# Kernel tuning notes

Measured on AMD Instinct MI355X. Metric: run time of the kernel, lower is better.

The kernel has to match this reference:

```python
import jax, jax.numpy as jnp
import numpy as np

V, H, E, I, K = 32000, 1024, 8, 4096, 2  # vocab, hidden, experts, intermediate, top-k
B, S = 4, 512


def setup_inputs() -> dict:
    key = jax.random.key(0)
    ks = jax.random.split(key, 11)
    s = 0.02
    return {
        "input_ids": jax.random.randint(ks[0], (B, S), 0, V),
        "emb": jax.random.normal(ks[1], (V, H), dtype=jnp.float32) * s,
        "router_w": jax.random.normal(ks[2], (H, E), dtype=jnp.float32) * s,
        "router_b": jnp.zeros((E,), jnp.float32),
        "w1": jax.random.normal(ks[3], (E, H, I), dtype=jnp.float32) * s,
        "b1": jnp.zeros((E, I), jnp.float32),
        "w2": jax.random.normal(ks[4], (E, I, H), dtype=jnp.float32) * s,
        "b2": jnp.zeros((E, H), jnp.float32),
        "lm_w": jax.random.normal(ks[5], (H, V), dtype=jnp.float32) * s,
        "lm_b": jnp.zeros((V,), jnp.float32),
    }


def reference(input_ids, emb, router_w, router_b, w1, b1, w2, b2, lm_w, lm_b):
    b, s = input_ids.shape
    x = emb[input_ids].reshape(-1, H)                      # [T, H], T = b*s
    router_logits = x @ router_w + router_b                # [T, E]
    routing_weights, selected_experts = jax.lax.top_k(router_logits, K)
    routing_weights = jax.nn.softmax(routing_weights, axis=-1)  # [T, K]
    # NOTE: original torch code accumulates UNWEIGHTED expert outputs
    # (routing_weights never multiply expert_output). Faithfully reproduced.
    # mask[t, e] = 1 if expert e is in token t's top-k (top_k indices are distinct)
    mask = jnp.any(selected_experts[:, :, None] == jnp.arange(E)[None, None, :], axis=1)
    mask = mask.astype(x.dtype)                            # [T, E]
    # Dense dispatch: run every expert FFN on all tokens, then mask-combine.
    h = jax.nn.gelu(jnp.einsum('th,ehi->tei', x, w1) + b1, approximate=False)  # [T,E,I]
    y = jnp.einsum('tei,eih->teh', h, w2) + b2             # [T, E, H]
    expert_out = jnp.einsum('te,teh->th', mask, y)         # [T, H]
    hidden = expert_out.reshape(b, s, H)
    logits = hidden @ lm_w + lm_b                          # [B, S, V]
    return logits, routing_weights, selected_experts
```

## Files before the change

### kernel.cpp

```cpp
#include <hip/hip_runtime.h>
#include <math.h>

#define TT 2048
#define HH 1024
#define EE 8
#define II 4096
#define VV 32000

typedef __attribute__((ext_vector_type(8))) short short8;
typedef __attribute__((ext_vector_type(4))) float f32x4;
typedef __attribute__((ext_vector_type(4))) unsigned short us4;

__device__ __forceinline__ unsigned short f2bf(float f) {
  union { float f; unsigned u; } v; v.f = f;
  unsigned r = (v.u + 0x7FFFu + ((v.u >> 16) & 1u)) >> 16;
  return (unsigned short)r;
}

__device__ __forceinline__ void gl2lds16(const void* g, void* l) {
  __builtin_amdgcn_global_load_lds(
      (__attribute__((address_space(1))) void*)(g),
      (__attribute__((address_space(3))) void*)(l),
      16, 0, 0);
}

__global__ __launch_bounds__(256) void k_transpose(
    const float* __restrict__ in, unsigned short* __restrict__ out,
    int R, int C, size_t ibs, size_t obs)
{
  __shared__ unsigned short tl[64][72];
  const int tid = threadIdx.x;
  const int c0 = blockIdx.x * 64;
  const int r0 = blockIdx.y * 64;
  const float* ip = in + (size_t)blockIdx.z * ibs;
  unsigned short* op = out + (size_t)blockIdx.z * obs;
  const int rl = tid >> 4;
  const int cc = (tid & 15) * 4;
#pragma unroll
  for (int p = 0; p < 4; p++) {
    const float4 v = *(const float4*)&ip[(size_t)(r0 + p*16 + rl)*C + c0 + cc];
    tl[cc+0][p*16+rl] = f2bf(v.x);
    tl[cc+1][p*16+rl] = f2bf(v.y);
    tl[cc+2][p*16+rl] = f2bf(v.z);
    tl[cc+3][p*16+rl] = f2bf(v.w);
  }
  __syncthreads();
  const int cl = tid >> 2;
  const int hc = (tid & 3) * 16;
  int4* dst = (int4*)&op[(size_t)(c0 + cl)*R + r0 + hc];
  dst[0] = *(int4*)&tl[cl][hc];
  dst[1] = *(int4*)&tl[cl][hc + 8];
}

__global__ __launch_bounds__(64) void k_gather_router(
    const int* __restrict__ ids, const float* __restrict__ emb,
    const float* __restrict__ rw, const float* __restrict__ rb,
    unsigned short* __restrict__ xb, float* __restrict__ rweights,
    float* __restrict__ sel, int* __restrict__ counts, int* __restrict__ tok_list,
    int* __restrict__ tinfo)
{
  const int t = blockIdx.x;
  const int lane = threadIdx.x;
  const int tok = ids[t];
  float p[EE];
#pragma unroll
  for (int e = 0; e < EE; e++) p[e] = 0.f;
#pragma unroll
  for (int c = 0; c < 4; c++) {
    const int h = c*256 + lane*4;
    const float4 xv = *(const float4*)&emb[tok*HH + h];
    us4 u;
    u[0] = f2bf(xv.x); u[1] = f2bf(xv.y); u[2] = f2bf(xv.z); u[3] = f2bf(xv.w);
    *(us4*)&xb[t*HH + h] = u;
    const float xs[4] = {xv.x, xv.y, xv.z, xv.w};
#pragma unroll
    for (int j = 0; j < 4; j++) {
      const float4 r0 = *(const float4*)&rw[(h+j)*EE];
      const float4 r1 = *(const float4*)&rw[(h+j)*EE + 4];
      p[0] += xs[j]*r0.x; p[1] += xs[j]*r0.y; p[2] += xs[j]*r0.z; p[3] += xs[j]*r0.w;
      p[4] += xs[j]*r1.x; p[5] += xs[j]*r1.y; p[6] += xs[j]*r1.z; p[7] += xs[j]*r1.w;
    }
  }
#pragma unroll
  for (int off = 32; off >= 1; off >>= 1) {
#pragma unroll
    for (int e = 0; e < EE; e++) p[e] += __shfl_xor(p[e], off, 64);
  }
  if (lane == 0) {
#pragma unroll
    for (int e = 0; e < EE; e++) p[e] += rb[e];
    int b0 = 0; float v0 = p[0];
#pragma unroll
    for (int e = 1; e < EE; e++) { if (p[e] > v0) { v0 = p[e]; b0 = e; } }
    int b1 = -1; float v1 = -3.0e38f;
#pragma unroll
    for (int e = 0; e < EE; e++) { if (e != b0 && p[e] > v1) { v1 = p[e]; b1 = e; } }
    const float ex = expf(v1 - v0);
    const float w0 = 1.f / (1.f + ex);
    const float w1v = ex * w0;
    rweights[t*2]   = w0;
    rweights[t*2+1] = w1v;
    sel[t*2]   = (float)b0;
    sel[t*2+1] = (float)b1;
    int j0 = atomicAdd(&counts[b0], 1); tok_list[b0*TT + j0] = t;
    int j1 = atomicAdd(&counts[b1], 1); tok_list[b1*TT + j1] = t;
    int4 ti; ti.x = b0; ti.y = j0; ti.z = b1; ti.w = j1;
    *(int4*)&tinfo[t*4] = ti;
  }
}

__global__ void k_scan(const int* __restrict__ counts, int* __restrict__ offsets) {
  int s = 0;
  for (int e = 0; e < EE; e++) { offsets[e] = s; s += counts[e]; }
}

__global__ __launch_bounds__(256) void k_ffn1(
    const unsigned short* __restrict__ xb, const unsigned short* __restrict__ w1t,
    const float* __restrict__ b1, const int* __restrict__ counts,
    const int* __restrict__ offsets, const int* __restrict__ tok_list,
    unsigned short* __restrict__ hbuf)
{
  const int e = blockIdx.z;
  const int Te = counts[e];
  const int m0 = blockIdx.y * 128;
  if (m0 >= Te) return;
  const int n0 = blockIdx.x * 128;

  __shared__ short As[128*32];
  __shared__ short Bs[128*32];
  const int tid = threadIdx.x;
  const int lane = tid & 63, wid = tid >> 6;
  const int wm = (wid & 1)*64, wn = (wid >> 1)*64;
  const int l15 = lane & 15, quad = lane >> 4;

  const int srow = tid >> 2, schk = (tid & 3) * 8;
  const int gr0 = m0 + srow, gr1 = gr0 + 64;
  const int tok0 = (gr0 < Te) ? tok_list[e*TT + gr0] : 0;
  const int tok1 = (gr1 < Te) ? tok_list[e*TT + gr1] : 0;
  const unsigned short* a0p = xb + (size_t)tok0*HH + schk;
  const unsigned short* a1p = xb + (size_t)tok1*HH + schk;
  const unsigned short* b0p = w1t + ((size_t)e*II + n0 + srow)*HH + schk;
  const unsigned short* b1p = b0p + (size_t)64*HH;
  short* aL0 = &As[(wid*16)*32];
  short* aL1 = &As[(64 + wid*16)*32];
  short* bL0 = &Bs[(wid*16)*32];
  short* bL1 = &Bs[(64 + wid*16)*32];

  f32x4 acc[4][4];
  const f32x4 zf = {0.f, 0.f, 0.f, 0.f};
#pragma unroll
  for (int i = 0; i < 4; i++)
#pragma unroll
    for (int j = 0; j < 4; j++) acc[i][j] = zf;

  for (int k0 = 0; k0 < HH; k0 += 32) {
    gl2lds16(a0p + k0, aL0);
    gl2lds16(a1p + k0, aL1);
    gl2lds16(b0p + k0, bL0);
    gl2lds16(b1p + k0, bL1);
    __syncthreads();
    short8 af[4], bfr[4];
#pragma unroll
    for (int i = 0; i < 4; i++) af[i]  = *(const short8*)&As[(wm + i*16 + l15)*32 + quad*8];
#pragma unroll
    for (int i = 0; i < 4; i++) bfr[i] = *(const short8*)&Bs[(wn + i*16 + l15)*32 + quad*8];
#pragma unroll
    for (int i = 0; i < 4; i++)
#pragma unroll
      for (int j = 0; j < 4; j++)
        acc[i][j] = __builtin_amdgcn_mfma_f32_16x16x32_bf16(af[i], bfr[j], acc[i][j], 0, 0, 0);
    __syncthreads();
  }

  const int base = offsets[e];
#pragma unroll
  for (int i = 0; i < 4; i++) {
#pragma unroll
    for (int j = 0; j < 4; j++) {
      const int col = n0 + wn + j*16 + l15;
      const float bb = b1[e*II + col];
#pragma unroll
      for (int r = 0; r < 4; r++) {
        const int rl = m0 + wm + i*16 + quad*4 + r;
        if (rl < Te) {
          float v = acc[i][j][r] + bb;
          v = 0.5f * v * (1.f + erff(v * 0.70710678118654752f));
          hbuf[(size_t)(base + rl)*II + col] = f2bf(v);
        }
      }
    }
  }
}

__global__ __launch_bounds__(256) void k_ffn2(
    const unsigned short* __restrict__ hbuf, const unsigned short* __restrict__ w2t,
    const float* __restrict__ b2, const int* __restrict__ counts,
    const int* __restrict__ offsets, float* __restrict__ ybuf)
{
  const int e = blockIdx.z;
  const int Te = counts[e];
  const int m0 = blockIdx.y * 128;
  if (m0 >= Te) return;
  const int n0 = blockIdx.x * 128;

  __shared__ short As[128*32];
  __shared__ short Bs[128*32];
  const int tid = threadIdx.x;
  const int lane = tid & 63, wid = tid >> 6;
  const int wm = (wid & 1)*64, wn = (wid >> 1)*64;
  const int l15 = lane & 15, quad = lane >> 4;

  const int srow = tid >> 2, schk = (tid & 3) * 8;
  const int base = offsets[e];
  int h0row = base + m0 + srow;      if (h0row > 2*TT - 1) h0row = 2*TT - 1;
  int h1row = base + m0 + 64 + srow; if (h1row > 2*TT - 1) h1row = 2*TT - 1;
  const unsigned short* a0p = hbuf + (size_t)h0row*II + schk;
  const unsigned short* a1p = hbuf + (size_t)h1row*II + schk;
  const unsigned short* b0p = w2t + ((size_t)e*HH + n0 + srow)*II + schk;
  const unsigned short* b1p = b0p + (size_t)64*II;
  short* aL0 = &As[(wid*16)*32];
  short* aL1 = &As[(64 + wid*16)*32];
  short* bL0 = &Bs[(wid*16)*32];
  short* bL1 = &Bs[(64 + wid*16)*32];

  f32x4 acc[4][4];
  const f32x4 zf = {0.f, 0.f, 0.f, 0.f};
#pragma unroll
  for (int i = 0; i < 4; i++)
#pragma unroll
    for (int j = 0; j < 4; j++) acc[i][j] = zf;

  for (int k0 = 0; k0 < II; k0 += 32) {
    gl2lds16(a0p + k0, aL0);
    gl2lds16(a1p + k0, aL1);
    gl2lds16(b0p + k0, bL0);
    gl2lds16(b1p + k0, bL1);
    __syncthreads();
    short8 af[4], bfr[4];
#pragma unroll
    for (int i = 0; i < 4; i++) af[i]  = *(const short8*)&As[(wm + i*16 + l15)*32 + quad*8];
#pragma unroll
    for (int i = 0; i < 4; i++) bfr[i] = *(const short8*)&Bs[(wn + i*16 + l15)*32 + quad*8];
#pragma unroll
    for (int i = 0; i < 4; i++)
#pragma unroll
      for (int j = 0; j < 4; j++)
        acc[i][j] = __builtin_amdgcn_mfma_f32_16x16x32_bf16(af[i], bfr[j], acc[i][j], 0, 0, 0);
    __syncthreads();
  }

#pragma unroll
  for (int i = 0; i < 4; i++) {
#pragma unroll
    for (int j = 0; j < 4; j++) {
      const int col = n0 + wn + j*16 + l15;
      const float bb = b2[e*HH + col];
#pragma unroll
      for (int r = 0; r < 4; r++) {
        const int rl = m0 + wm + i*16 + quad*4 + r;
        if (rl < Te) ybuf[(size_t)(base + rl)*HH + col] = acc[i][j][r] + bb;
      }
    }
  }
}

__global__ __launch_bounds__(256) void k_combine(
    const float* __restrict__ ybuf, const int* __restrict__ offsets,
    const int* __restrict__ tinfo, unsigned short* __restrict__ xoutb)
{
  const int t = blockIdx.x;
  const int4 ti = *(const int4*)&tinfo[t*4];
  const int s0 = offsets[ti.x] + ti.y;
  const int s1 = offsets[ti.z] + ti.w;
  const int i = threadIdx.x * 4;
  const float4 a = *(const float4*)&ybuf[(size_t)s0*HH + i];
  const float4 b = *(const float4*)&ybuf[(size_t)s1*HH + i];
  us4 u;
  u[0] = f2bf(a.x + b.x); u[1] = f2bf(a.y + b.y);
  u[2] = f2bf(a.z + b.z); u[3] = f2bf(a.w + b.w);
  *(us4*)&xoutb[(size_t)t*HH + i] = u;
}

__global__ __launch_bounds__(256) void k_lmhead(
    const unsigned short* __restrict__ A, const unsigned short* __restrict__ lmwt,
    const float* __restrict__ bias, float* __restrict__ out)
{
  __shared__ short As[128*32];
  __shared__ short Bs[128*32];
  const int tid = threadIdx.x;
  const int m0 = blockIdx.x*128, n0 = blockIdx.y*128;
  const int lane = tid & 63, wid = tid >> 6;
  const int wm = (wid & 1)*64, wn = (wid >> 1)*64;
  const int l15 = lane & 15, quad = lane >> 4;

  const int srow = tid >> 2, schk = (tid & 3) * 8;
  const unsigned short* a0p = A + (size_t)(m0 + srow)*HH + schk;
  const unsigned short* a1p = a0p + (size_t)64*HH;
  const unsigned short* b0p = lmwt + (size_t)(n0 + srow)*HH + schk;
  const unsigned short* b1p = b0p + (size_t)64*HH;
  short* aL0 = &As[(wid*16)*32];
  short* aL1 = &As[(64 + wid*16)*32];
  short* bL0 = &Bs[(wid*16)*32];
  short* bL1 = &Bs[(64 + wid*16)*32];

  f32x4 acc[4][4];
  const f32x4 zf = {0.f, 0.f, 0.f, 0.f};
#pragma unroll
  for (int i = 0; i < 4; i++)
#pragma unroll
    for (int j = 0; j < 4; j++) acc[i][j] = zf;

  for (int k0 = 0; k0 < HH; k0 += 32) {
    gl2lds16(a0p + k0, aL0);
    gl2lds16(a1p + k0, aL1);
    gl2lds16(b0p + k0, bL0);
    gl2lds16(b1p + k0, bL1);
    __syncthreads();
    short8 af[4], bfr[4];
#pragma unroll
    for (int i = 0; i < 4; i++) af[i]  = *(const short8*)&As[(wm + i*16 + l15)*32 + quad*8];
#pragma unroll
    for (int i = 0; i < 4; i++) bfr[i] = *(const short8*)&Bs[(wn + i*16 + l15)*32 + quad*8];
#pragma unroll
    for (int i = 0; i < 4; i++)
#pragma unroll
      for (int j = 0; j < 4; j++)
        acc[i][j] = __builtin_amdgcn_mfma_f32_16x16x32_bf16(af[i], bfr[j], acc[i][j], 0, 0, 0);
    __syncthreads();
  }

#pragma unroll
  for (int i = 0; i < 4; i++) {
#pragma unroll
    for (int j = 0; j < 4; j++) {
      const int col = n0 + wn + j*16 + l15;
      const float bb = bias[col];
#pragma unroll
      for (int r = 0; r < 4; r++) {
        const int row = m0 + wm + i*16 + quad*4 + r;
        out[(size_t)row*VV + col] = acc[i][j][r] + bb;
      }
    }
  }
}

extern "C" void kernel_launch(void* const* d_in, const int* in_sizes, int n_in,
                              void* d_out, int out_size, void* d_ws, size_t ws_size,
                              hipStream_t stream) {
  const int*   ids = (const int*)d_in[0];
  const float* emb = (const float*)d_in[1];
  const float* rw  = (const float*)d_in[2];
  const float* rb  = (const float*)d_in[3];
  const float* w1  = (const float*)d_in[4];
  const float* b1  = (const float*)d_in[5];
  const float* w2  = (const float*)d_in[6];
  const float* b2  = (const float*)d_in[7];
  const float* lmw = (const float*)d_in[8];
  const float* lmb = (const float*)d_in[9];

  char* ws = (char*)d_ws;
  unsigned short* xb    = (unsigned short*)(ws);
  unsigned short* xoutb = (unsigned short*)(ws + 4194304);
  unsigned short* lmwt  = (unsigned short*)(ws + 8388608);
  int* counts   = (int*)(ws + 8388608 + 65536000);
  int* offsets  = counts + 16;
  int* tinfo    = counts + 32;
  int* tok_list = tinfo + TT*4;

  char* ob = (char*)d_out;
  float* logits   = (float*)ob;
  float* rweights = (float*)(ob + (size_t)TT*VV*4);
  float* sel      = rweights + TT*2;
  unsigned short* w1t  = (unsigned short*)(ob);
  unsigned short* w2t  = (unsigned short*)(ob + 67108864);
  unsigned short* hbuf = (unsigned short*)(ob + 134217728);
  float*          ybuf = (float*)(ob + 167772160);

  hipMemsetAsync(counts, 0, 64, stream);

  k_gather_router<<<TT, 64, 0, stream>>>(ids, emb, rw, rb, xb, rweights, sel,
                                         counts, tok_list, tinfo);
  k_scan<<<1, 1, 0, stream>>>(counts, offsets);

  k_transpose<<<dim3(II/64, HH/64, EE), 256, 0, stream>>>(w1, w1t, HH, II,
                                                          (size_t)HH*II, (size_t)HH*II);
  k_transpose<<<dim3(HH/64, II/64, EE), 256, 0, stream>>>(w2, w2t, II, HH,
                                                          (size_t)II*HH, (size_t)II*HH);
  k_transpose<<<dim3(VV/64, HH/64, 1), 256, 0, stream>>>(lmw, lmwt, HH, VV, 0, 0);

  k_ffn1<<<dim3(II/128, TT/128, EE), 256, 0, stream>>>(xb, w1t, b1, counts, offsets,
                                                       tok_list, hbuf);
  k_ffn2<<<dim3(HH/128, TT/128, EE), 256, 0, stream>>>(hbuf, w2t, b2, counts, offsets, ybuf);
  k_combine<<<TT, 256, 0, stream>>>(ybuf, offsets, tinfo, xoutb);
  k_lmhead<<<dim3(TT/128, VV/128), 256, 0, stream>>>(xoutb, lmwt, lmb, logits);
}
```

Measured before the change: 1.041 ms.

## Double-buffer GEMM LDS tiles, split-K the second FFN, enlarge LM-head tiles

Adds double-buffered LDS staging to the FFN1, FFN2 and LM-head GEMMs so the next K-tile is loaded while MFMA runs on the current one. FFN2 is split into four K chunks to give it more blocks. Each chunk writes its partial sums to a separate slab, and the combine kernel adds the slabs and the bias. The LM head moves to 256x128 tiles with 512 threads and an XCD-aware block swizzle to improve reuse. The costs are doubled LDS use, extra partial-sum memory traffic, and the assumption that the workspace can hold four ybuf slabs.

```diff
diff --git a/kernel.cpp b/kernel.cpp
--- a/kernel.cpp
+++ b/kernel.cpp
@@ -126,14 +126,14 @@
   if (m0 >= Te) return;
   const int n0 = blockIdx.x * 128;
 
-  __shared__ short As[128*32];
-  __shared__ short Bs[128*32];
+  __shared__ short As[2][128*32];
+  __shared__ short Bs[2][128*32];
   const int tid = threadIdx.x;
   const int lane = tid & 63, wid = tid >> 6;
   const int wm = (wid & 1)*64, wn = (wid >> 1)*64;
   const int l15 = lane & 15, quad = lane >> 4;
-
   const int srow = tid >> 2, schk = (tid & 3) * 8;
+
   const int gr0 = m0 + srow, gr1 = gr0 + 64;
   const int tok0 = (gr0 < Te) ? tok_list[e*TT + gr0] : 0;
   const int tok1 = (gr1 < Te) ? tok_list[e*TT + gr1] : 0;
@@ -141,10 +141,7 @@
   const unsigned short* a1p = xb + (size_t)tok1*HH + schk;
   const unsigned short* b0p = w1t + ((size_t)e*II + n0 + srow)*HH + schk;
   const unsigned short* b1p = b0p + (size_t)64*HH;
-  short* aL0 = &As[(wid*16)*32];
-  short* aL1 = &As[(64 + wid*16)*32];
-  short* bL0 = &Bs[(wid*16)*32];
-  short* bL1 = &Bs[(64 + wid*16)*32];
+  const int w16 = (wid*16)*32;
 
   f32x4 acc[4][4];
   const f32x4 zf = {0.f, 0.f, 0.f, 0.f};
@@ -153,24 +150,40 @@
 #pragma unroll
     for (int j = 0; j < 4; j++) acc[i][j] = zf;
 
-  for (int k0 = 0; k0 < HH; k0 += 32) {
-    gl2lds16(a0p + k0, aL0);
-    gl2lds16(a1p + k0, aL1);
-    gl2lds16(b0p + k0, bL0);
-    gl2lds16(b1p + k0, bL1);
-    __syncthreads();
+  short* Ac = &As[0][0]; short* An = &As[1][0];
+  short* Bc = &Bs[0][0]; short* Bn = &Bs[1][0];
+
+  auto compute = [&](const short* Ab, const short* Bb) {
     short8 af[4], bfr[4];
 #pragma unroll
-    for (int i = 0; i < 4; i++) af[i]  = *(const short8*)&As[(wm + i*16 + l15)*32 + quad*8];
-#pragma unroll
-    for (int i = 0; i < 4; i++) bfr[i] = *(const short8*)&Bs[(wn + i*16 + l15)*32 + quad*8];
+    for (int i = 0; i < 4; i++) af[i]  = *(const short8*)&Ab[(wm + i*16 + l15)*32 + quad*8];
+#pragma unroll
+    for (int i = 0; i < 4; i++) bfr[i] = *(const short8*)&Bb[(wn + i*16 + l15)*32 + quad*8];
 #pragma unroll
     for (int i = 0; i < 4; i++)
 #pragma unroll
       for (int j = 0; j < 4; j++)
         acc[i][j] = __builtin_amdgcn_mfma_f32_16x16x32_bf16(af[i], bfr[j], acc[i][j], 0, 0, 0);
+  };
+
+  gl2lds16(a0p, Ac + w16);
+  gl2lds16(a1p, Ac + 64*32 + w16);
+  gl2lds16(b0p, Bc + w16);
+  gl2lds16(b1p, Bc + 64*32 + w16);
+  __syncthreads();
+
+  for (int t = 0; t < 31; t++) {
+    const int kn = (t + 1) * 32;
+    gl2lds16(a0p + kn, An + w16);
+    gl2lds16(a1p + kn, An + 64*32 + w16);
+    gl2lds16(b0p + kn, Bn + w16);
+    gl2lds16(b1p + kn, Bn + 64*32 + w16);
+    compute(Ac, Bc);
     __syncthreads();
-  }
+    short* tp = Ac; Ac = An; An = tp;
+    tp = Bc; Bc = Bn; Bn = tp;
+  }
+  compute(Ac, Bc);
 
   const int base = offsets[e];
 #pragma unroll
@@ -194,34 +207,31 @@
 
 __global__ __launch_bounds__(256) void k_ffn2(
     const unsigned short* __restrict__ hbuf, const unsigned short* __restrict__ w2t,
-    const float* __restrict__ b2, const int* __restrict__ counts,
-    const int* __restrict__ offsets, float* __restrict__ ybuf)
-{
-  const int e = blockIdx.z;
+    const int* __restrict__ counts, const int* __restrict__ offsets,
+    float* __restrict__ ybuf)
+{
+  const int e = blockIdx.z >> 2, kc = blockIdx.z & 3;
   const int Te = counts[e];
   const int m0 = blockIdx.y * 128;
   if (m0 >= Te) return;
   const int n0 = blockIdx.x * 128;
 
-  __shared__ short As[128*32];
-  __shared__ short Bs[128*32];
+  __shared__ short As[2][128*32];
+  __shared__ short Bs[2][128*32];
   const int tid = threadIdx.x;
   const int lane = tid & 63, wid = tid >> 6;
   const int wm = (wid & 1)*64, wn = (wid >> 1)*64;
   const int l15 = lane & 15, quad = lane >> 4;
-
   const int srow = tid >> 2, schk = (tid & 3) * 8;
+
   const int base = offsets[e];
   int h0row = base + m0 + srow;      if (h0row > 2*TT - 1) h0row = 2*TT - 1;
   int h1row = base + m0 + 64 + srow; if (h1row > 2*TT - 1) h1row = 2*TT - 1;
-  const unsigned short* a0p = hbuf + (size_t)h0row*II + schk;
-  const unsigned short* a1p = hbuf + (size_t)h1row*II + schk;
-  const unsigned short* b0p = w2t + ((size_t)e*HH + n0 + srow)*II + schk;
+  const unsigned short* a0p = hbuf + (size_t)h0row*II + kc*1024 + schk;
+  const unsigned short* a1p = hbuf + (size_t)h1row*II + kc*1024 + schk;
+  const unsigned short* b0p = w2t + ((size_t)e*HH + n0 + srow)*II + kc*1024 + schk;
   const unsigned short* b1p = b0p + (size_t)64*II;
-  short* aL0 = &As[(wid*16)*32];
-  short* aL1 = &As[(64 + wid*16)*32];
-  short* bL0 = &Bs[(wid*16)*32];
-  short* bL1 = &Bs[(64 + wid*16)*32];
+  const int w16 = (wid*16)*32;
 
   f32x4 acc[4][4];
   const f32x4 zf = {0.f, 0.f, 0.f, 0.f};
@@ -230,78 +240,101 @@
 #pragma unroll
     for (int j = 0; j < 4; j++) acc[i][j] = zf;
 
-  for (int k0 = 0; k0 < II; k0 += 32) {
-    gl2lds16(a0p + k0, aL0);
-    gl2lds16(a1p + k0, aL1);
-    gl2lds16(b0p + k0, bL0);
-    gl2lds16(b1p + k0, bL1);
-    __syncthreads();
+  short* Ac = &As[0][0]; short* An = &As[1][0];
+  short* Bc = &Bs[0][0]; short* Bn = &Bs[1][0];
+
+  auto compute = [&](const short* Ab, const short* Bb) {
     short8 af[4], bfr[4];
 #pragma unroll
-    for (int i = 0; i < 4; i++) af[i]  = *(const short8*)&As[(wm + i*16 + l15)*32 + quad*8];
-#pragma unroll
-    for (int i = 0; i < 4; i++) bfr[i] = *(const short8*)&Bs[(wn + i*16 + l15)*32 + quad*8];
+    for (int i = 0; i < 4; i++) af[i]  = *(const short8*)&Ab[(wm + i*16 + l15)*32 + quad*8];
+#pragma unroll
+    for (int i = 0; i < 4; i++) bfr[i] = *(const short8*)&Bb[(wn + i*16 + l15)*32 + quad*8];
 #pragma unroll
     for (int i = 0; i < 4; i++)
 #pragma unroll
       for (int j = 0; j < 4; j++)
         acc[i][j] = __builtin_amdgcn_mfma_f32_16x16x32_bf16(af[i], bfr[j], acc[i][j], 0, 0, 0);
+  };
+
+  gl2lds16(a0p, Ac + w16);
+  gl2lds16(a1p, Ac + 64*32 + w16);
+  gl2lds16(b0p, Bc + w16);
+  gl2lds16(b1p, Bc + 64*32 + w16);
+  __syncthreads();
+
+  for (int t = 0; t < 31; t++) {
+    const int kn = (t + 1) * 32;
+    gl2lds16(a0p + kn, An + w16);
+    gl2lds16(a1p + kn, An + 64*32 + w16);
+    gl2lds16(b0p + kn, Bn + w16);
+    gl2lds16(b1p + kn, Bn + 64*32 + w16);
+    compute(Ac, Bc);
     __syncthreads();
-  }
-
+    short* tp = Ac; Ac = An; An = tp;
+    tp = Bc; Bc = Bn; Bn = tp;
+  }
+  compute(Ac, Bc);
+
+  float* yp = ybuf + (size_t)kc * 2*TT*HH;
 #pragma unroll
   for (int i = 0; i < 4; i++) {
 #pragma unroll
     for (int j = 0; j < 4; j++) {
       const int col = n0 + wn + j*16 + l15;
-      const float bb = b2[e*HH + col];
 #pragma unroll
       for (int r = 0; r < 4; r++) {
         const int rl = m0 + wm + i*16 + quad*4 + r;
-        if (rl < Te) ybuf[(size_t)(base + rl)*HH + col] = acc[i][j][r] + bb;
+        if (rl < Te) yp[(size_t)(base + rl)*HH + col] = acc[i][j][r];
       }
     }
   }
 }
 
 __global__ __launch_bounds__(256) void k_combine(
-    const float* __restrict__ ybuf, const int* __restrict__ offsets,
-    const int* __restrict__ tinfo, unsigned short* __restrict__ xoutb)
+    const float* __restrict__ ybuf, const float* __restrict__ b2,
+    const int* __restrict__ offsets, const int* __restrict__ tinfo,
+    unsigned short* __restrict__ xoutb)
 {
   const int t = blockIdx.x;
   const int4 ti = *(const int4*)&tinfo[t*4];
-  const int s0 = offsets[ti.x] + ti.y;
-  const int s1 = offsets[ti.z] + ti.w;
+  const size_t s0 = (size_t)(offsets[ti.x] + ti.y) * HH;
+  const size_t s1 = (size_t)(offsets[ti.z] + ti.w) * HH;
   const int i = threadIdx.x * 4;
-  const float4 a = *(const float4*)&ybuf[(size_t)s0*HH + i];
-  const float4 b = *(const float4*)&ybuf[(size_t)s1*HH + i];
+  const float4 c0 = *(const float4*)&b2[ti.x*HH + i];
+  const float4 c1 = *(const float4*)&b2[ti.z*HH + i];
+  float sx = c0.x + c1.x, sy = c0.y + c1.y, sz = c0.z + c1.z, sw = c0.w + c1.w;
+  const size_t SLAB = (size_t)2*TT*HH;
+#pragma unroll
+  for (int kc = 0; kc < 4; kc++) {
+    const float4 a = *(const float4*)&ybuf[kc*SLAB + s0 + i];
+    const float4 b = *(const float4*)&ybuf[kc*SLAB + s1 + i];
+    sx += a.x + b.x; sy += a.y + b.y; sz += a.z + b.z; sw += a.w + b.w;
+  }
   us4 u;
-  u[0] = f2bf(a.x + b.x); u[1] = f2bf(a.y + b.y);
-  u[2] = f2bf(a.z + b.z); u[3] = f2bf(a.w + b.w);
+  u[0] = f2bf(sx); u[1] = f2bf(sy); u[2] = f2bf(sz); u[3] = f2bf(sw);
   *(us4*)&xoutb[(size_t)t*HH + i] = u;
 }
 
-__global__ __launch_bounds__(256) void k_lmhead(
+__global__ __launch_bounds__(512) void k_lmhead(
     const unsigned short* __restrict__ A, const unsigned short* __restrict__ lmwt,
     const float* __restrict__ bias, float* __restrict__ out)
 {
-  __shared__ short As[128*32];
-  __shared__ short Bs[128*32];
+  __shared__ short As[2][256*32];
+  __shared__ short Bs[2][128*32];
+  const int b = blockIdx.x;
+  const int logical = (b & 7) * 250 + (b >> 3);
+  const int m0 = (logical & 7) << 8;
+  const int n0 = (logical >> 3) << 7;
   const int tid = threadIdx.x;
-  const int m0 = blockIdx.x*128, n0 = blockIdx.y*128;
   const int lane = tid & 63, wid = tid >> 6;
-  const int wm = (wid & 1)*64, wn = (wid >> 1)*64;
+  const int wm = (wid & 3)*64, wn = (wid >> 2)*64;
   const int l15 = lane & 15, quad = lane >> 4;
-
   const int srow = tid >> 2, schk = (tid & 3) * 8;
+
   const unsigned short* a0p = A + (size_t)(m0 + srow)*HH + schk;
-  const unsigned short* a1p = a0p + (size_t)64*HH;
+  const unsigned short* a1p = a0p + (size_t)128*HH;
   const unsigned short* b0p = lmwt + (size_t)(n0 + srow)*HH + schk;
-  const unsigned short* b1p = b0p + (size_t)64*HH;
-  short* aL0 = &As[(wid*16)*32];
-  short* aL1 = &As[(64 + wid*16)*32];
-  short* bL0 = &Bs[(wid*16)*32];
-  short* bL1 = &Bs[(64 + wid*16)*32];
+  const int w16 = (wid*16)*32;
 
   f32x4 acc[4][4];
   const f32x4 zf = {0.f, 0.f, 0.f, 0.f};
@@ -310,24 +343,38 @@
 #pragma unroll
     for (int j = 0; j < 4; j++) acc[i][j] = zf;
 
-  for (int k0 = 0; k0 < HH; k0 += 32) {
-    gl2lds16(a0p + k0, aL0);
-    gl2lds16(a1p + k0, aL1);
-    gl2lds16(b0p + k0, bL0);
-    gl2lds16(b1p + k0, bL1);
-    __syncthreads();
+  short* Ac = &As[0][0]; short* An = &As[1][0];
+  short* Bc = &Bs[0][0]; short* Bn = &Bs[1][0];
+
+  auto compute = [&](const short* Ab, const short* Bb) {
     short8 af[4], bfr[4];
 #pragma unroll
-    for (int i = 0; i < 4; i++) af[i]  = *(const short8*)&As[(wm + i*16 + l15)*32 + quad*8];
-#pragma unroll
-    for (int i = 0; i < 4; i++) bfr[i] = *(const short8*)&Bs[(wn + i*16 + l15)*32 + quad*8];
+    for (int i = 0; i < 4; i++) af[i]  = *(const short8*)&Ab[(wm + i*16 + l15)*32 + quad*8];
+#pragma unroll
+    for (int i = 0; i < 4; i++) bfr[i] = *(const short8*)&Bb[(wn + i*16 + l15)*32 + quad*8];
 #pragma unroll
     for (int i = 0; i < 4; i++)
 #pragma unroll
       for (int j = 0; j < 4; j++)
         acc[i][j] = __builtin_amdgcn_mfma_f32_16x16x32_bf16(af[i], bfr[j], acc[i][j], 0, 0, 0);
+  };
+
+  gl2lds16(a0p, Ac + w16);
+  gl2lds16(a1p, Ac + 128*32 + w16);
+  gl2lds16(b0p, Bc + w16);
+  __syncthreads();
+
+  for (int t = 0; t < 31; t++) {
+    const int kn = (t + 1) * 32;
+    gl2lds16(a0p + kn, An + w16);
+    gl2lds16(a1p + kn, An + 128*32 + w16);
+    gl2lds16(b0p + kn, Bn + w16);
+    compute(Ac, Bc);
     __syncthreads();
-  }
+    short* tp = Ac; Ac = An; An = tp;
+    tp = Bc; Bc = Bn; Bn = tp;
+  }
+  compute(Ac, Bc);
 
 #pragma unroll
   for (int i = 0; i < 4; i++) {
@@ -390,7 +437,7 @@
 
   k_ffn1<<<dim3(II/128, TT/128, EE), 256, 0, stream>>>(xb, w1t, b1, counts, offsets,
                                                        tok_list, hbuf);
-  k_ffn2<<<dim3(HH/128, TT/128, EE), 256, 0, stream>>>(hbuf, w2t, b2, counts, offsets, ybuf);
-  k_combine<<<TT, 256, 0, stream>>>(ybuf, offsets, tinfo, xoutb);
-  k_lmhead<<<dim3(TT/128, VV/128), 256, 0, stream>>>(xoutb, lmwt, lmb, logits);
-}
+  k_ffn2<<<dim3(HH/128, TT/128, EE*4), 256, 0, stream>>>(hbuf, w2t, counts, offsets, ybuf);
+  k_combine<<<TT, 256, 0, stream>>>(ybuf, b2, offsets, tinfo, xoutb);
+  k_lmhead<<<(TT/256)*(VV/128), 512, 0, stream>>>(xoutb, lmwt, lmb, logits);
+}
```

Result: faster. 970.8 us (-6.7%).
